# Performance work log

Hardware: AMD Instinct MI355X
Metric: run time of the kernel (lower is better)

Reference implementation:

```python
import jax, jax.numpy as jnp
import numpy as np

T_STEPS = 2048
N = 4096


def setup_inputs() -> dict:
    key = jax.random.key(0)
    ks = jax.random.split(key, 3)
    ones = jnp.ones((N,), jnp.float32)
    w_mean, w_var = 0.55, 0.65
    w = w_mean - w_var + 2.0 * w_var * jax.random.uniform(ks[0], (N, N), jnp.float32)
    E_L = -60.0 * ones
    return {
        'x_in': jax.random.normal(ks[1], (T_STEPS, N), jnp.float32),
        'w': w,
        'E_L': E_L,
        'C_m': 1.0 * ones,
        'G': 0.7 * ones,
        'R_I': 18.0 * ones,
        'f_v': 0.15 * ones,
        'f_I': 0.3 * ones,
        'delta_theta_s': 30.0 * ones,
        'b_s': 0.3 * ones,
        'a_v': 0.5 * ones,
        'b_v': 0.5 * ones,
        'theta_inf': -20.0 * ones,
        'delta_V': 12.0 * ones,
        'I_A': 1.0 * ones,
        'v0': E_L,                 # v initialized to E_L
        'theta_s0': 30.0 * ones,   # theta_s init
        'theta_v0': 1.0 * ones,    # theta_v init
        'I_add0': jnp.zeros((N,), jnp.float32),
    }


def reference(x_in, w, E_L, C_m, G, R_I, f_v, f_I, delta_theta_s, b_s,
              a_v, b_v, theta_inf, delta_V, I_A, v0, theta_s0, theta_v0, I_add0):
    def step(carry, x_t):
        v, theta_s, theta_v, I_add = carry
        I = x_t + w @ I_add                       # [N] recurrent matvec
        dv = (I * R_I - G * (v - E_L)) / C_m
        v_next = v + dv
        thr = theta_s + theta_v
        spiked_soft = jax.nn.sigmoid(v_next - thr)          # surrogate spike
        spiked = (v_next >= thr).astype(v.dtype)            # hard spike
        not_spiked = 1.0 - spiked
        v_reset = E_L + f_v * (v - E_L) - delta_V
        v_new = spiked * v_reset + not_spiked * v_next
        theta_s_new = (1.0 - b_s) * theta_s + spiked * delta_theta_s
        d_theta_v = a_v * (v_new - E_L) - b_v * (theta_v - theta_inf)
        theta_v_new = theta_v + not_spiked * d_theta_v
        I_add_new = (1.0 - f_I) * I_add + spiked_soft * I_A
        return (v_new, theta_s_new, theta_v_new, I_add_new), (v_new, spiked_soft)

    _, (v_seq, s_seq) = jax.lax.scan(step, (v0, theta_s0, theta_v0, I_add0), x_in)
    return jnp.stack([v_seq, s_seq])  # [2, T, N]
```

## Files before the change

kernel.cpp:

```cpp
#include <hip/hip_runtime.h>
#include <hip/hip_cooperative_groups.h>

namespace cg = cooperative_groups;

constexpr int N    = 4096;
constexpr int T    = 2048;
constexpr int NBLK = 256;
constexpr int NTHR = 512;
constexpr int ROWS_PER_WG   = 16;
constexpr int ROWS_PER_WAVE = 2;

struct Params {
    const float *x_in, *w, *E_L, *C_m, *G, *R_I, *f_v, *f_I, *dts, *b_s,
                *a_v, *b_v, *tinf, *dV, *I_A, *v0, *ts0, *tv0, *ia0;
    float *out;
    unsigned *flags;
    float *ia_buf;
};

#define DOT(wv, iv) ((wv).x*(iv).x + (wv).y*(iv).y + (wv).z*(iv).z + (wv).w*(iv).w)
#define AGLD(ptr) __hip_atomic_load(ptr, __ATOMIC_RELAXED, __HIP_MEMORY_SCOPE_AGENT)
#define AGST(ptr, val) __hip_atomic_store(ptr, val, __ATOMIC_RELAXED, __HIP_MEMORY_SCOPE_AGENT)

__global__ __launch_bounds__(NTHR, 2)
void glif_persistent(Params p)
{
    cg::grid_group grid = cg::this_grid();
    __shared__ float ia_lds[2][N];

    const int tid  = threadIdx.x;
    const int wg   = blockIdx.x;
    const int wave = tid >> 6;
    const int lane = tid & 63;
    const int row0 = wg * ROWS_PER_WG + wave * ROWS_PER_WAVE;
    const int prow = row0 + (lane != 0);

    const float c_EL = p.E_L[prow],  c_Cm = p.C_m[prow], c_G   = p.G[prow];
    const float c_RI = p.R_I[prow],  c_fv = p.f_v[prow], c_fI  = p.f_I[prow];
    const float c_dts = p.dts[prow], c_bs = p.b_s[prow], c_av  = p.a_v[prow];
    const float c_bv  = p.b_v[prow], c_tinf = p.tinf[prow];
    const float c_dV  = p.dV[prow],  c_IA = p.I_A[prow];
    float v  = p.v0[prow], ts = p.ts0[prow], tv = p.tv0[prow];
    float ia = p.ia0[prow];

    const float4* wrA = (const float4*)(p.w + (size_t)(row0 + 0) * N);
    const float4* wrB = (const float4*)(p.w + (size_t)(row0 + 1) * N);
    const float4 a0r = wrA[lane+0],   a1r = wrA[lane+64],  a2r = wrA[lane+128],
                 a3r = wrA[lane+192], a4r = wrA[lane+256], a5r = wrA[lane+320],
                 a6r = wrA[lane+384], a7r = wrA[lane+448], a8r = wrA[lane+512],
                 a9r = wrA[lane+576], aAr = wrA[lane+640], aBr = wrA[lane+704],
                 aCr = wrA[lane+768], aDr = wrA[lane+832], aEr = wrA[lane+896],
                 aFr = wrA[lane+960];
    const float4 b0r = wrB[lane+0],   b1r = wrB[lane+64],  b2r = wrB[lane+128],
                 b3r = wrB[lane+192], b4r = wrB[lane+256], b5r = wrB[lane+320],
                 b6r = wrB[lane+384], b7r = wrB[lane+448], b8r = wrB[lane+512],
                 b9r = wrB[lane+576], bAr = wrB[lane+640], bBr = wrB[lane+704],
                 bCr = wrB[lane+768], bDr = wrB[lane+832], bEr = wrB[lane+896],
                 bFr = wrB[lane+960];

    if (tid == 0) AGST(&p.flags[wg], 0u);
    ((float4*)ia_lds[0])[tid]        = ((const float4*)p.ia0)[tid];
    ((float4*)ia_lds[0])[tid + NTHR] = ((const float4*)p.ia0)[tid + NTHR];
    grid.sync();

    float x = p.x_in[prow];

    for (int t = 0; t < T; ++t) {
        const float4* lds4 = (const float4*)ia_lds[t & 1];

        float sA = 0.f, sB = 0.f;
        { float4 q = lds4[lane+  0]; sA += DOT(a0r,q); sB += DOT(b0r,q); }
        { float4 q = lds4[lane+ 64]; sA += DOT(a1r,q); sB += DOT(b1r,q); }
        { float4 q = lds4[lane+128]; sA += DOT(a2r,q); sB += DOT(b2r,q); }
        { float4 q = lds4[lane+192]; sA += DOT(a3r,q); sB += DOT(b3r,q); }
        { float4 q = lds4[lane+256]; sA += DOT(a4r,q); sB += DOT(b4r,q); }
        { float4 q = lds4[lane+320]; sA += DOT(a5r,q); sB += DOT(b5r,q); }
        { float4 q = lds4[lane+384]; sA += DOT(a6r,q); sB += DOT(b6r,q); }
        { float4 q = lds4[lane+448]; sA += DOT(a7r,q); sB += DOT(b7r,q); }
        { float4 q = lds4[lane+512]; sA += DOT(a8r,q); sB += DOT(b8r,q); }
        { float4 q = lds4[lane+576]; sA += DOT(a9r,q); sB += DOT(b9r,q); }
        { float4 q = lds4[lane+640]; sA += DOT(aAr,q); sB += DOT(bAr,q); }
        { float4 q = lds4[lane+704]; sA += DOT(aBr,q); sB += DOT(bBr,q); }
        { float4 q = lds4[lane+768]; sA += DOT(aCr,q); sB += DOT(bCr,q); }
        { float4 q = lds4[lane+832]; sA += DOT(aDr,q); sB += DOT(bDr,q); }
        { float4 q = lds4[lane+896]; sA += DOT(aEr,q); sB += DOT(bEr,q); }
        { float4 q = lds4[lane+960]; sA += DOT(aFr,q); sB += DOT(bFr,q); }

        #pragma unroll
        for (int m = 32; m >= 1; m >>= 1) {
            sA += __shfl_xor(sA, m, 64);
            sB += __shfl_xor(sB, m, 64);
        }

        float a      = (lane == 0) ? sA : sB;
        float I      = x + a;
        float dv     = (I * c_RI - c_G * (v - c_EL)) / c_Cm;
        float v_next = v + dv;
        float thr    = ts + tv;
        float ssoft  = 1.f / (1.f + __expf(thr - v_next));
        float ia_new = (1.f - c_fI) * ia + ssoft * c_IA;

        float* dst = p.ia_buf + (size_t)((t + 1) & 1) * N;
        if (lane < 2) AGST(&dst[prow], ia_new);

        __syncthreads();

        const bool notlast = (t + 1 < T);
        const unsigned tgt = (unsigned)(t + 1);

        if (wave == 0 && lane == 0 && notlast)
            AGST(&p.flags[wg], tgt);

        {
            bool  sp      = (v_next >= thr);
            float v_reset = c_EL + c_fv * (v - c_EL) - c_dV;
            float v_new   = sp ? v_reset : v_next;
            float ts_new  = (1.f - c_bs) * ts + (sp ? c_dts : 0.f);
            float dtv     = c_av * (v_new - c_EL) - c_bv * (tv - c_tinf);
            float tv_new  = tv + (sp ? 0.f : dtv);
            v = v_new; ts = ts_new; tv = tv_new; ia = ia_new;
            if (lane < 2) {
                p.out[(size_t)t * N + prow] = v_new;
                p.out[(size_t)T * N + (size_t)t * N + prow] = ssoft;
                if (notlast) x = p.x_in[(size_t)(t + 1) * N + prow];
            }
        }

        if (notlast) {
            if (wave == 0) {
                const unsigned long long* f64 =
                    (const unsigned long long*)p.flags;
                bool d0 = false, d1 = false;
                for (;;) {
                    if (!d0) {
                        unsigned long long q = AGLD(&f64[lane]);
                        d0 = ((unsigned)q >= tgt) & ((unsigned)(q >> 32) >= tgt);
                    }
                    if (!d1) {
                        unsigned long long q = AGLD(&f64[lane + 64]);
                        d1 = ((unsigned)q >= tgt) & ((unsigned)(q >> 32) >= tgt);
                    }
                    if (__all(d0 && d1)) break;
                    __builtin_amdgcn_s_sleep(1);
                }
            }
            __syncthreads();

            const unsigned long long* src64 =
                (const unsigned long long*)(p.ia_buf + (size_t)((t + 1) & 1) * N);
            unsigned long long q0 = AGLD(&src64[tid            ]);
            unsigned long long q1 = AGLD(&src64[tid + NTHR     ]);
            unsigned long long q2 = AGLD(&src64[tid + 2 * NTHR ]);
            unsigned long long q3 = AGLD(&src64[tid + 3 * NTHR ]);
            unsigned long long* l64 = (unsigned long long*)ia_lds[(t + 1) & 1];
            l64[tid           ] = q0;
            l64[tid + NTHR    ] = q1;
            l64[tid + 2 * NTHR] = q2;
            l64[tid + 3 * NTHR] = q3;

            __syncthreads();
        }
    }
}

extern "C" void kernel_launch(void* const* d_in, const int* in_sizes, int n_in,
                              void* d_out, int out_size, void* d_ws, size_t ws_size,
                              hipStream_t stream)
{
    Params p;
    p.x_in = (const float*)d_in[0];
    p.w    = (const float*)d_in[1];
    p.E_L  = (const float*)d_in[2];
    p.C_m  = (const float*)d_in[3];
    p.G    = (const float*)d_in[4];
    p.R_I  = (const float*)d_in[5];
    p.f_v  = (const float*)d_in[6];
    p.f_I  = (const float*)d_in[7];
    p.dts  = (const float*)d_in[8];
    p.b_s  = (const float*)d_in[9];
    p.a_v  = (const float*)d_in[10];
    p.b_v  = (const float*)d_in[11];
    p.tinf = (const float*)d_in[12];
    p.dV   = (const float*)d_in[13];
    p.I_A  = (const float*)d_in[14];
    p.v0   = (const float*)d_in[15];
    p.ts0  = (const float*)d_in[16];
    p.tv0  = (const float*)d_in[17];
    p.ia0  = (const float*)d_in[18];
    p.out  = (float*)d_out;
    p.flags  = (unsigned*)d_ws;
    p.ia_buf = (float*)((char*)d_ws + 4096);

    void* args[] = { &p };
    hipLaunchCooperativeKernel((const void*)glif_persistent,
                               dim3(NBLK), dim3(NTHR), args, 0, stream);
}
```

Before: 6.719 ms.

## Repartition matvec: 1024 threads each own a column slice across 16 rows

Each workgroup now runs 1024 threads, and each thread holds one float4 column slice for all 16 of the workgroup's rows. This replaces the per-wave two-row layout. The recurrent vector slice is loaded straight from global memory into registers, so the LDS staging copy of the full 4096-element state vector and one barrier per step are gone. Per-row partial sums are reduced across waves through a small LDS array, and wave 0 alone does the neuron update, the publish and the flag spin. The trade is 16 butterfly shuffle reductions per wave instead of 2, and occupancy drops to one workgroup per CU.

After: 13.68 ms. +103.6%, slower.

```diff
diff --git a/kernel.cpp b/kernel.cpp
--- a/kernel.cpp
+++ b/kernel.cpp
@@ -6,9 +6,8 @@
 constexpr int N    = 4096;
 constexpr int T    = 2048;
 constexpr int NBLK = 256;
-constexpr int NTHR = 512;
-constexpr int ROWS_PER_WG   = 16;
-constexpr int ROWS_PER_WAVE = 2;
+constexpr int NTHR = 1024;
+constexpr int ROWS_PER_WG = 16;
 
 struct Params {
     const float *x_in, *w, *E_L, *C_m, *G, *R_I, *f_v, *f_I, *dts, *b_s,
@@ -22,112 +21,118 @@
 #define AGLD(ptr) __hip_atomic_load(ptr, __ATOMIC_RELAXED, __HIP_MEMORY_SCOPE_AGENT)
 #define AGST(ptr, val) __hip_atomic_store(ptr, val, __ATOMIC_RELAXED, __HIP_MEMORY_SCOPE_AGENT)
 
-__global__ __launch_bounds__(NTHR, 2)
+__global__ __launch_bounds__(NTHR, 1)
 void glif_persistent(Params p)
 {
     cg::grid_group grid = cg::this_grid();
-    __shared__ float ia_lds[2][N];
+    __shared__ float part[16 * 16];
 
     const int tid  = threadIdx.x;
     const int wg   = blockIdx.x;
     const int wave = tid >> 6;
     const int lane = tid & 63;
-    const int row0 = wg * ROWS_PER_WG + wave * ROWS_PER_WAVE;
-    const int prow = row0 + (lane != 0);
 
-    const float c_EL = p.E_L[prow],  c_Cm = p.C_m[prow], c_G   = p.G[prow];
-    const float c_RI = p.R_I[prow],  c_fv = p.f_v[prow], c_fI  = p.f_I[prow];
-    const float c_dts = p.dts[prow], c_bs = p.b_s[prow], c_av  = p.a_v[prow];
-    const float c_bv  = p.b_v[prow], c_tinf = p.tinf[prow];
-    const float c_dV  = p.dV[prow],  c_IA = p.I_A[prow];
-    float v  = p.v0[prow], ts = p.ts0[prow], tv = p.tv0[prow];
-    float ia = p.ia0[prow];
+    const int lrow = (lane < 15) ? lane : 15;
+    const int srow = wg * ROWS_PER_WG + lrow;
 
-    const float4* wrA = (const float4*)(p.w + (size_t)(row0 + 0) * N);
-    const float4* wrB = (const float4*)(p.w + (size_t)(row0 + 1) * N);
-    const float4 a0r = wrA[lane+0],   a1r = wrA[lane+64],  a2r = wrA[lane+128],
-                 a3r = wrA[lane+192], a4r = wrA[lane+256], a5r = wrA[lane+320],
-                 a6r = wrA[lane+384], a7r = wrA[lane+448], a8r = wrA[lane+512],
-                 a9r = wrA[lane+576], aAr = wrA[lane+640], aBr = wrA[lane+704],
-                 aCr = wrA[lane+768], aDr = wrA[lane+832], aEr = wrA[lane+896],
-                 aFr = wrA[lane+960];
-    const float4 b0r = wrB[lane+0],   b1r = wrB[lane+64],  b2r = wrB[lane+128],
-                 b3r = wrB[lane+192], b4r = wrB[lane+256], b5r = wrB[lane+320],
-                 b6r = wrB[lane+384], b7r = wrB[lane+448], b8r = wrB[lane+512],
-                 b9r = wrB[lane+576], bAr = wrB[lane+640], bBr = wrB[lane+704],
-                 bCr = wrB[lane+768], bDr = wrB[lane+832], bEr = wrB[lane+896],
-                 bFr = wrB[lane+960];
+    const float c_EL = p.E_L[srow],  c_Cm = p.C_m[srow], c_G   = p.G[srow];
+    const float c_RI = p.R_I[srow],  c_fv = p.f_v[srow], c_fI  = p.f_I[srow];
+    const float c_dts = p.dts[srow], c_bs = p.b_s[srow], c_av  = p.a_v[srow];
+    const float c_bv  = p.b_v[srow], c_tinf = p.tinf[srow];
+    const float c_dV  = p.dV[srow],  c_IA = p.I_A[srow];
+    float v  = p.v0[srow], ts = p.ts0[srow], tv = p.tv0[srow];
+    float ia_self = p.ia0[srow];
+
+    const float4* w4 = (const float4*)p.w;
+    const size_t rb  = (size_t)wg * ROWS_PER_WG * (N / 4) + tid;
+    const float4 w0  = w4[rb +  0 * (N/4)], w1  = w4[rb +  1 * (N/4)],
+                 w2  = w4[rb +  2 * (N/4)], w3  = w4[rb +  3 * (N/4)],
+                 w4r = w4[rb +  4 * (N/4)], w5  = w4[rb +  5 * (N/4)],
+                 w6  = w4[rb +  6 * (N/4)], w7  = w4[rb +  7 * (N/4)],
+                 w8  = w4[rb +  8 * (N/4)], w9  = w4[rb +  9 * (N/4)],
+                 w10 = w4[rb + 10 * (N/4)], w11 = w4[rb + 11 * (N/4)],
+                 w12 = w4[rb + 12 * (N/4)], w13 = w4[rb + 13 * (N/4)],
+                 w14 = w4[rb + 14 * (N/4)], w15 = w4[rb + 15 * (N/4)];
 
     if (tid == 0) AGST(&p.flags[wg], 0u);
-    ((float4*)ia_lds[0])[tid]        = ((const float4*)p.ia0)[tid];
-    ((float4*)ia_lds[0])[tid + NTHR] = ((const float4*)p.ia0)[tid + NTHR];
+    float4 iav = ((const float4*)p.ia0)[tid];
     grid.sync();
 
-    float x = p.x_in[prow];
+    float x = p.x_in[srow];
 
     for (int t = 0; t < T; ++t) {
-        const float4* lds4 = (const float4*)ia_lds[t & 1];
+        float p0  = DOT(w0 , iav), p1  = DOT(w1 , iav),
+              p2  = DOT(w2 , iav), p3  = DOT(w3 , iav),
+              p4  = DOT(w4r, iav), p5  = DOT(w5 , iav),
+              p6  = DOT(w6 , iav), p7  = DOT(w7 , iav),
+              p8  = DOT(w8 , iav), p9  = DOT(w9 , iav),
+              p10 = DOT(w10, iav), p11 = DOT(w11, iav),
+              p12 = DOT(w12, iav), p13 = DOT(w13, iav),
+              p14 = DOT(w14, iav), p15 = DOT(w15, iav);
 
-        float sA = 0.f, sB = 0.f;
-        { float4 q = lds4[lane+  0]; sA += DOT(a0r,q); sB += DOT(b0r,q); }
-        { float4 q = lds4[lane+ 64]; sA += DOT(a1r,q); sB += DOT(b1r,q); }
-        { float4 q = lds4[lane+128]; sA += DOT(a2r,q); sB += DOT(b2r,q); }
-        { float4 q = lds4[lane+192]; sA += DOT(a3r,q); sB += DOT(b3r,q); }
-        { float4 q = lds4[lane+256]; sA += DOT(a4r,q); sB += DOT(b4r,q); }
-        { float4 q = lds4[lane+320]; sA += DOT(a5r,q); sB += DOT(b5r,q); }
-        { float4 q = lds4[lane+384]; sA += DOT(a6r,q); sB += DOT(b6r,q); }
-        { float4 q = lds4[lane+448]; sA += DOT(a7r,q); sB += DOT(b7r,q); }
-        { float4 q = lds4[lane+512]; sA += DOT(a8r,q); sB += DOT(b8r,q); }
-        { float4 q = lds4[lane+576]; sA += DOT(a9r,q); sB += DOT(b9r,q); }
-        { float4 q = lds4[lane+640]; sA += DOT(aAr,q); sB += DOT(bAr,q); }
-        { float4 q = lds4[lane+704]; sA += DOT(aBr,q); sB += DOT(bBr,q); }
-        { float4 q = lds4[lane+768]; sA += DOT(aCr,q); sB += DOT(bCr,q); }
-        { float4 q = lds4[lane+832]; sA += DOT(aDr,q); sB += DOT(bDr,q); }
-        { float4 q = lds4[lane+896]; sA += DOT(aEr,q); sB += DOT(bEr,q); }
-        { float4 q = lds4[lane+960]; sA += DOT(aFr,q); sB += DOT(bFr,q); }
+        #define BFLY(m) \
+            p0  += __shfl_xor(p0 , m, 64); p1  += __shfl_xor(p1 , m, 64); \
+            p2  += __shfl_xor(p2 , m, 64); p3  += __shfl_xor(p3 , m, 64); \
+            p4  += __shfl_xor(p4 , m, 64); p5  += __shfl_xor(p5 , m, 64); \
+            p6  += __shfl_xor(p6 , m, 64); p7  += __shfl_xor(p7 , m, 64); \
+            p8  += __shfl_xor(p8 , m, 64); p9  += __shfl_xor(p9 , m, 64); \
+            p10 += __shfl_xor(p10, m, 64); p11 += __shfl_xor(p11, m, 64); \
+            p12 += __shfl_xor(p12, m, 64); p13 += __shfl_xor(p13, m, 64); \
+            p14 += __shfl_xor(p14, m, 64); p15 += __shfl_xor(p15, m, 64);
+        BFLY(32) BFLY(16) BFLY(8) BFLY(4) BFLY(2) BFLY(1)
+        #undef BFLY
 
-        #pragma unroll
-        for (int m = 32; m >= 1; m >>= 1) {
-            sA += __shfl_xor(sA, m, 64);
-            sB += __shfl_xor(sB, m, 64);
+        if (lane == 0) {
+            part[ 0*16 + wave] = p0;  part[ 1*16 + wave] = p1;
+            part[ 2*16 + wave] = p2;  part[ 3*16 + wave] = p3;
+            part[ 4*16 + wave] = p4;  part[ 5*16 + wave] = p5;
+            part[ 6*16 + wave] = p6;  part[ 7*16 + wave] = p7;
+            part[ 8*16 + wave] = p8;  part[ 9*16 + wave] = p9;
+            part[10*16 + wave] = p10; part[11*16 + wave] = p11;
+            part[12*16 + wave] = p12; part[13*16 + wave] = p13;
+            part[14*16 + wave] = p14; part[15*16 + wave] = p15;
         }
-
-        float a      = (lane == 0) ? sA : sB;
-        float I      = x + a;
-        float dv     = (I * c_RI - c_G * (v - c_EL)) / c_Cm;
-        float v_next = v + dv;
-        float thr    = ts + tv;
-        float ssoft  = 1.f / (1.f + __expf(thr - v_next));
-        float ia_new = (1.f - c_fI) * ia + ssoft * c_IA;
-
-        float* dst = p.ia_buf + (size_t)((t + 1) & 1) * N;
-        if (lane < 2) AGST(&dst[prow], ia_new);
-
         __syncthreads();
 
         const bool notlast = (t + 1 < T);
-        const unsigned tgt = (unsigned)(t + 1);
+        float* dst = p.ia_buf + (size_t)((t + 1) & 1) * N;
 
-        if (wave == 0 && lane == 0 && notlast)
-            AGST(&p.flags[wg], tgt);
+        if (wave == 0) {
+            const int rr = lane & 15;
+            float4 r0 = *(const float4*)&part[rr * 16 +  0];
+            float4 r1 = *(const float4*)&part[rr * 16 +  4];
+            float4 r2 = *(const float4*)&part[rr * 16 +  8];
+            float4 r3 = *(const float4*)&part[rr * 16 + 12];
+            float a = (r0.x + r0.y + r0.z + r0.w) + (r1.x + r1.y + r1.z + r1.w)
+                    + (r2.x + r2.y + r2.z + r2.w) + (r3.x + r3.y + r3.z + r3.w);
 
-        {
+            float I      = x + a;
+            float dv     = (I * c_RI - c_G * (v - c_EL)) / c_Cm;
+            float v_next = v + dv;
+            float thr    = ts + tv;
+            float ssoft  = 1.f / (1.f + __expf(thr - v_next));
+            float ia_new = (1.f - c_fI) * ia_self + ssoft * c_IA;
+
+            if (lane < 16) AGST(&dst[srow], ia_new);
+            asm volatile("s_waitcnt vmcnt(0)" ::: "memory");
+            if (lane == 0 && notlast)
+                AGST(&p.flags[wg], (unsigned)(t + 1));
+
             bool  sp      = (v_next >= thr);
             float v_reset = c_EL + c_fv * (v - c_EL) - c_dV;
             float v_new   = sp ? v_reset : v_next;
             float ts_new  = (1.f - c_bs) * ts + (sp ? c_dts : 0.f);
             float dtv     = c_av * (v_new - c_EL) - c_bv * (tv - c_tinf);
             float tv_new  = tv + (sp ? 0.f : dtv);
-            v = v_new; ts = ts_new; tv = tv_new; ia = ia_new;
-            if (lane < 2) {
-                p.out[(size_t)t * N + prow] = v_new;
-                p.out[(size_t)T * N + (size_t)t * N + prow] = ssoft;
-                if (notlast) x = p.x_in[(size_t)(t + 1) * N + prow];
+            v = v_new; ts = ts_new; tv = tv_new; ia_self = ia_new;
+            if (lane < 16) {
+                p.out[(size_t)t * N + srow] = v_new;
+                p.out[(size_t)T * N + (size_t)t * N + srow] = ssoft;
+                if (notlast) x = p.x_in[(size_t)(t + 1) * N + srow];
             }
-        }
 
-        if (notlast) {
-            if (wave == 0) {
+            if (notlast) {
+                const unsigned tgt = (unsigned)(t + 1);
                 const unsigned long long* f64 =
                     (const unsigned long long*)p.flags;
                 bool d0 = false, d1 = false;
@@ -144,21 +149,17 @@
                     __builtin_amdgcn_s_sleep(1);
                 }
             }
-            __syncthreads();
+        }
+        __syncthreads();
 
-            const unsigned long long* src64 =
-                (const unsigned long long*)(p.ia_buf + (size_t)((t + 1) & 1) * N);
-            unsigned long long q0 = AGLD(&src64[tid            ]);
-            unsigned long long q1 = AGLD(&src64[tid + NTHR     ]);
-            unsigned long long q2 = AGLD(&src64[tid + 2 * NTHR ]);
-            unsigned long long q3 = AGLD(&src64[tid + 3 * NTHR ]);
-            unsigned long long* l64 = (unsigned long long*)ia_lds[(t + 1) & 1];
-            l64[tid           ] = q0;
-            l64[tid + NTHR    ] = q1;
-            l64[tid + 2 * NTHR] = q2;
-            l64[tid + 3 * NTHR] = q3;
-
-            __syncthreads();
+        if (notlast) {
+            const unsigned long long* s64 = (const unsigned long long*)dst;
+            unsigned long long qa = AGLD(&s64[2 * tid + 0]);
+            unsigned long long qb = AGLD(&s64[2 * tid + 1]);
+            iav.x = __uint_as_float((unsigned)qa);
+            iav.y = __uint_as_float((unsigned)(qa >> 32));
+            iav.z = __uint_as_float((unsigned)qb);
+            iav.w = __uint_as_float((unsigned)(qb >> 32));
         }
     }
 }
```
